# Kernel tuning notes

Hardware: AMD Instinct MI355X
Metric: run time of the kernel (lower is better)

## Reference

```python
import jax, jax.numpy as jnp
import numpy as np

EMBED_DIM = 1024
NUM_HEADS = 16
HEAD_DIM = EMBED_DIM // NUM_HEADS


def setup_inputs() -> dict:
    key = jax.random.key(0)
    k_x, k_wqkv, k_bqkv, k_wo, k_bo = jax.random.split(key, 5)
    B, T, C = 4, 2048, EMBED_DIM
    # PyTorch Linear default init scale ~ 1/sqrt(fan_in); use small normals
    s = 1.0 / np.sqrt(C)
    return {
        "x": jax.random.normal(k_x, (B, T, C), dtype=jnp.float32),
        "w_qkv": jax.random.normal(k_wqkv, (C, 3 * C), dtype=jnp.float32) * s,
        "b_qkv": jax.random.normal(k_bqkv, (3 * C,), dtype=jnp.float32) * s,
        "w_out": jax.random.normal(k_wo, (C, C), dtype=jnp.float32) * s,
        "b_out": jax.random.normal(k_bo, (C,), dtype=jnp.float32) * s,
    }


def reference(x, w_qkv, b_qkv, w_out, b_out):
    B, T, C = x.shape
    H, D = NUM_HEADS, HEAD_DIM
    qkv = x @ w_qkv + b_qkv                      # (B, T, 3C)
    q, k, v = jnp.split(qkv, 3, axis=-1)
    # (B, H, T, D)
    q = q.reshape(B, T, H, D).transpose(0, 2, 1, 3)
    k = k.reshape(B, T, H, D).transpose(0, 2, 1, 3)
    v = v.reshape(B, T, H, D).transpose(0, 2, 1, 3)
    scores = jnp.einsum("bhqd,bhkd->bhqk", q, k) / jnp.sqrt(jnp.float32(D))
    causal = jnp.tril(jnp.ones((T, T), dtype=bool))  # (T, T)
    scores = jnp.where(causal[None, None, :, :], scores, -jnp.inf)
    attn = jax.nn.softmax(scores, axis=-1)
    out = jnp.einsum("bhqk,bhkd->bhqd", attn, v)  # (B, H, T, D)
    out = out.transpose(0, 2, 1, 3).reshape(B, T, C)
    return out @ w_out + b_out
```

## Files before the change

kernel.cpp:

```cpp
#include <hip/hip_runtime.h>
#include <hip/hip_bf16.h>

#define B_  4
#define T_  2048
#define C_  1024
#define H_  16
#define D_  64
#define BH_ (B_*H_)

typedef float  f32x4  __attribute__((ext_vector_type(4)));
typedef __bf16 bf16x8 __attribute__((ext_vector_type(8)));
typedef __bf16 bf16x2 __attribute__((ext_vector_type(2)));

static __device__ __forceinline__ ushort f2bf(float f) {
    union { float f; unsigned u; } x; x.f = f;
    unsigned r = ((x.u >> 16) & 1u) + 0x7fffu;
    return (ushort)((x.u + r) >> 16);
}

static __device__ __forceinline__ uint packbf(float a, float b) {
    bf16x2 v = { (__bf16)a, (__bf16)b };
    return __builtin_bit_cast(uint, v);
}

static __device__ __forceinline__ void gload_lds16(const void* g, void* l) {
    __builtin_amdgcn_global_load_lds(
        (const __attribute__((address_space(1))) unsigned int*)g,
        (__attribute__((address_space(3))) unsigned int*)l, 16, 0, 0);
}

template<int N> static __device__ __forceinline__ void waitcnt_vm() {
    if constexpr (N == 0) asm volatile("s_waitcnt vmcnt(0)" ::: "memory");
    else if constexpr (N == 3) asm volatile("s_waitcnt vmcnt(3)" ::: "memory");
    else static_assert(N == 0 || N == 3);
    __builtin_amdgcn_sched_barrier(0);
}
static __device__ __forceinline__ void lgkm0() {
    asm volatile("s_waitcnt lgkmcnt(0)" ::: "memory");
    __builtin_amdgcn_sched_barrier(0);
}

__global__ __launch_bounds__(256) void prep_kernel(
    const float* __restrict__ x,     ushort* __restrict__ xb,
    const float* __restrict__ wqkv,  ushort* __restrict__ wqkvT,
    const float* __restrict__ wout,  ushort* __restrict__ woutT)
{
    __shared__ float tile[32][33];
    const int bid = blockIdx.x;
    if (bid < 8192) {
        int i = (bid * 256 + threadIdx.x) * 4;
        float4 v = *(const float4*)(x + i);
        ushort4 o;
        o.x = f2bf(v.x); o.y = f2bf(v.y); o.z = f2bf(v.z); o.w = f2bf(v.w);
        *(ushort4*)(xb + i) = o;
        return;
    }
    const float* in; ushort* out; int K, N, t;
    if (bid < 8192 + 3072) { t = bid - 8192;        in = wqkv; out = wqkvT; K = 1024; N = 3072; }
    else                   { t = bid - 8192 - 3072; in = wout; out = woutT; K = 1024; N = 1024; }
    const int nbx = N / 32;
    const int n0 = (t % nbx) * 32, k0 = (t / nbx) * 32;
    const int tx = threadIdx.x & 31, ty = threadIdx.x >> 5;
    #pragma unroll
    for (int r = 0; r < 32; r += 8)
        tile[ty + r][tx] = in[(size_t)(k0 + ty + r) * N + n0 + tx];
    __syncthreads();
    #pragma unroll
    for (int r = 0; r < 32; r += 8)
        out[(size_t)(n0 + ty + r) * K + k0 + tx] = f2bf(tile[tx][ty + r]);
}

template<int MFR, int NFR, bool QKV>
__global__ __launch_bounds__(512, 2) void gemm_hk(
    const ushort* __restrict__ A,
    const ushort* __restrict__ Bt,
    const float*  __restrict__ bias,
    void* __restrict__ outp,
    ushort* __restrict__ vtp)
{
    constexpr int NT    = 16;
    constexpr int BM    = MFR * 32;
    constexpr int BN    = NFR * 64;
    constexpr int APASS = BM / 128;
    constexpr int LB    = BN / 128;
    constexpr int ABUF  = BM * 128;
    constexpr int BBUF  = BN * 128;
    constexpr int PK    = APASS + LB;
    __shared__ __align__(16) char lds[2 * ABUF + 2 * BBUF];
    char* ldsB = lds + 2 * ABUF;

    const int gX   = gridDim.x;
    const int orig = blockIdx.y * gX + blockIdx.x;
    const int cpx  = (gX * gridDim.y) >> 3;
    const int wg   = (orig & 7) * cpx + (orig >> 3);
    const int m0 = (wg / gX) * BM, n0 = (wg % gX) * BN;

    const int tid = threadIdx.x, lane = tid & 63;
    const int wv = tid >> 6, wm = wv >> 2, wn = wv & 3;
    const int lr = lane & 15, lh = lane >> 4;

    const int sc = (tid & 3) ^ ((tid >> 2) & 3);
    const ushort* aA = A  + (size_t)(m0 + (tid >> 2)) * 1024 + sc * 8;
    const ushort* aB = Bt + (size_t)(n0 + (tid >> 2)) * 1024 + sc * 8;

    const int cxor = (lh ^ (lr & 3)) * 16;
    const int arow = (wm * (MFR * 16) + lr) * 64 + cxor;
    const int brow = (wn * (NFR * 16) + lr) * 64 + cxor;

    f32x4 acc[MFR][NFR] = {};

    auto stage_a = [&](int buf, int t, int kh) {
        #pragma unroll
        for (int p = 0; p < APASS; ++p)
            gload_lds16(aA + (size_t)p * 131072 + t * 64 + kh * 32,
                        lds + buf * ABUF + kh * (ABUF / 2) + p * 8192 + tid * 16);
    };
    auto stage_b = [&](int buf, int t, int kh) {
        #pragma unroll
        for (int p = 0; p < LB; ++p)
            gload_lds16(aB + (size_t)p * 131072 + t * 64 + kh * 32,
                        ldsB + buf * BBUF + kh * (BBUF / 2) + p * 8192 + tid * 16);
    };
    auto read_a = [&](bf16x8 (&af)[MFR], int buf, int kh) {
        const char* base = lds + buf * ABUF + kh * (ABUF / 2) + arow;
        #pragma unroll
        for (int mi = 0; mi < MFR; ++mi) af[mi] = *(const bf16x8*)(base + mi * 1024);
    };
    auto read_b = [&](bf16x8& b0, bf16x8& b1, int buf, int kh, int nh) {
        const char* base = ldsB + buf * BBUF + kh * (BBUF / 2) + brow + nh * 2048;
        b0 = *(const bf16x8*)(base);
        b1 = *(const bf16x8*)(base + 1024);
    };

#define MFMA2(NI, BB0, BB1)                                                          \
    do {                                                                             \
        __builtin_amdgcn_s_setprio(1);                                               \
        _Pragma("unroll")                                                            \
        for (int mi = 0; mi < MFR; ++mi) {                                           \
            acc[mi][NI]     = __builtin_amdgcn_mfma_f32_16x16x32_bf16(af[mi], BB0,   \
                                                     acc[mi][NI], 0, 0, 0);          \
            acc[mi][NI + 1] = __builtin_amdgcn_mfma_f32_16x16x32_bf16(af[mi], BB1,   \
                                                     acc[mi][NI + 1], 0, 0, 0);      \
        }                                                                            \
        __builtin_amdgcn_s_setprio(0);                                               \
    } while (0)

    stage_a(0, 0, 0); stage_b(0, 0, 0);
    stage_a(0, 0, 1); stage_b(0, 0, 1);
    waitcnt_vm<PK>();
    __builtin_amdgcn_s_barrier();

    for (int t = 0; t < NT; ++t) {
        const int cur = t & 1, nxt = cur ^ 1;
        const bool pf = (t + 1 < NT);
        bf16x8 af[MFR], b0, b1;
        read_a(af, cur, 0); read_b(b0, b1, cur, 0, 0);
        if (pf) { stage_a(nxt, t + 1, 0); stage_b(nxt, t + 1, 0); }
        if (t < NT - 1) waitcnt_vm<PK>(); else waitcnt_vm<0>();
        __builtin_amdgcn_s_barrier();
        lgkm0();
        MFMA2(0, b0, b1);
        read_a(af, cur, 1); read_b(b0, b1, cur, 1, 0);
        if (pf) { stage_a(nxt, t + 1, 1); stage_b(nxt, t + 1, 1); }
        if (t < NT - 1) waitcnt_vm<PK>();
        __builtin_amdgcn_s_barrier();
        lgkm0();
        MFMA2(0, b0, b1);
    }
#undef MFMA2

    #pragma unroll
    for (int mi = 0; mi < MFR; ++mi) {
        #pragma unroll
        for (int ni = 0; ni < NFR; ++ni) {
            int col = n0 + wn * (NFR * 16) + ni * 16 + lr;
            float bv = bias[col];
            if constexpr (QKV) {
                ushort* qkv = (ushort*)outp;
                int which = col >> 10;
                int h = (col & 1023) >> 6;
                int d = col & 63;
                if (which == 2) {
                    #pragma unroll
                    for (int r = 0; r < 4; ++r) {
                        int row = m0 + wm * (MFR * 16) + mi * 16 + lh * 4 + r;
                        int b = row >> 11, tt = row & 2047;
                        vtp[(((size_t)(b * H_ + h)) * D_ + d) * T_ + tt] =
                            f2bf(acc[mi][ni][r] + bv);
                    }
                } else {
                    #pragma unroll
                    for (int r = 0; r < 4; ++r) {
                        int row = m0 + wm * (MFR * 16) + mi * 16 + lh * 4 + r;
                        int b = row >> 11, tt = row & 2047;
                        float v = acc[mi][ni][r] + bv;
                        if (which == 0) v *= 0.18033688011112042f;
                        qkv[(size_t)which * (BH_ * T_ * D_) +
                            (((size_t)(b * H_ + h)) * T_ + tt) * D_ + d] = f2bf(v);
                    }
                }
            } else {
                float* Cout = (float*)outp;
                #pragma unroll
                for (int r = 0; r < 4; ++r) {
                    int row = m0 + wm * (MFR * 16) + mi * 16 + lh * 4 + r;
                    Cout[(size_t)row * C_ + col] = acc[mi][ni][r] + bv;
                }
            }
        }
    }
}

__global__ __launch_bounds__(256, 4) void flash_kernel(
    const ushort* __restrict__ qb,
    const ushort* __restrict__ kb,
    const ushort* __restrict__ vt,
    ushort* __restrict__ ob)
{
    __shared__ __align__(16) ushort sK[2][64 * 64];
    __shared__ __align__(16) ushort sV[2][64 * 64];
    const int wg  = ((blockIdx.x & 7) << 7) | (blockIdx.x >> 3);
    const int bh  = wg >> 4;
    const int pr  = wg & 15;
    const int qtA = pr, qtB = 31 - pr;
    const int lane = threadIdx.x & 63, wv = threadIdx.x >> 6;
    const int lr = lane & 15, lh = lane >> 4;

    const ushort* qrowA = qb + ((size_t)bh * T_ + qtA * 64 + wv * 16 + lr) * D_;
    const ushort* qrowB = qb + ((size_t)bh * T_ + qtB * 64 + wv * 16 + lr) * D_;
    bf16x8 qfA0 = *(const bf16x8*)(qrowA + lh * 8);
    bf16x8 qfA1 = *(const bf16x8*)(qrowA + 32 + lh * 8);
    bf16x8 qfB0 = *(const bf16x8*)(qrowB + lh * 8);
    bf16x8 qfB1 = *(const bf16x8*)(qrowB + 32 + lh * 8);

    const int srow = lane >> 3;
    const int scol = ((lane & 7) ^ srow) * 8;
    const ushort* kbase = kb + (size_t)bh * T_ * D_;
    const ushort* vbase = vt + (size_t)bh * D_ * T_;

    const int swv  = (lr & 7) << 4;
    const int off0 = (16 * lh) ^ swv;
    const int off1 = (64 + 16 * lh) ^ swv;

    f32x4 oA[4] = {}, oB[4] = {};
    float mA = -1e30f, lA = 0.f, mB = -1e30f, lB = 0.f;

    auto redmax = [&](float x) {
        x = fmaxf(x, __int_as_float(__builtin_amdgcn_ds_swizzle(__float_as_int(x), 0x401F)));
        x = fmaxf(x, __shfl_xor(x, 32, 64));
        return x;
    };
    auto redsum = [&](float x) {
        x += __int_as_float(__builtin_amdgcn_ds_swizzle(__float_as_int(x), 0x401F));
        x += __shfl_xor(x, 32, 64);
        return x;
    };

    auto maskS = [&](f32x4 (&s)[4]) {
        #pragma unroll
        for (int nt = 0; nt < 4; ++nt) {
            const int kb0 = 8 * lh + 4 * (nt & 1) + 32 * (nt >> 1);
            #pragma unroll
            for (int r = 0; r < 4; ++r)
                if (kb0 + r > wv * 16 + lr) s[nt][r] = -INFINITY;
        }
    };

    auto softmax_pv = [&](f32x4 (&s)[4], float& mrow, float& lsum, f32x4 (&o)[4],
                          const char* V0) {
        float t0 = fmaxf(fmaxf(s[0][0], s[0][1]), s[0][2]);
        float t1 = fmaxf(fmaxf(s[0][3], s[1][0]), s[1][1]);
        float t2 = fmaxf(fmaxf(s[1][2], s[1][3]), s[2][0]);
        float t3 = fmaxf(fmaxf(s[2][1], s[2][2]), s[2][3]);
        float t4 = fmaxf(fmaxf(s[3][0], s[3][1]), s[3][2]);
        float u0 = fmaxf(fmaxf(t0, t1), t2);
        float u1 = fmaxf(fmaxf(t3, t4), s[3][3]);
        float lmax = fmaxf(u0, u1);
        if (__any(lmax > mrow + 8.f)) {
            float pmax = redmax(lmax);
            float mnew = fmaxf(mrow, pmax);
            float al = __builtin_exp2f(mrow - mnew);
            lsum *= al;
            #pragma unroll
            for (int r = 0; r < 4; ++r) {
                float ar = __shfl(al, lh * 20 + r, 64);
                o[0][r] *= ar; o[1][r] *= ar; o[2][r] *= ar; o[3][r] *= ar;
            }
            mrow = mnew;
        }
        float rsum = 0.f;
        uint pk[8];
        #pragma unroll
        for (int nt = 0; nt < 4; ++nt) {
            float p0 = __builtin_exp2f(s[nt][0] - mrow);
            float p1 = __builtin_exp2f(s[nt][1] - mrow);
            float p2 = __builtin_exp2f(s[nt][2] - mrow);
            float p3 = __builtin_exp2f(s[nt][3] - mrow);
            rsum += (p0 + p1) + (p2 + p3);
            pk[nt * 2]     = packbf(p0, p1);
            pk[nt * 2 + 1] = packbf(p2, p3);
        }
        lsum += rsum;
        uint4 w0 = {pk[0], pk[1], pk[2], pk[3]};
        uint4 w1 = {pk[4], pk[5], pk[6], pk[7]};
        bf16x8 pf0 = __builtin_bit_cast(bf16x8, w0);
        bf16x8 pf1 = __builtin_bit_cast(bf16x8, w1);
        __builtin_amdgcn_s_setprio(1);
        #pragma unroll
        for (int dt = 0; dt < 4; ++dt) {
            const char* vrow = V0 + (dt * 16 + lr) * 128;
            bf16x8 v0 = *(const bf16x8*)(vrow + off0);
            bf16x8 v1 = *(const bf16x8*)(vrow + off1);
            o[dt] = __builtin_amdgcn_mfma_f32_16x16x32_bf16(pf0, v0, o[dt], 0, 0, 0);
            o[dt] = __builtin_amdgcn_mfma_f32_16x16x32_bf16(pf1, v1, o[dt], 0, 0, 0);
        }
        __builtin_amdgcn_s_setprio(0);
    };

    #pragma unroll
    for (int i = 0; i < 2; ++i) {
        int j = i * 4 + wv;
        gload_lds16(kbase + (size_t)(j * 8 + srow) * D_ + scol, &sK[0][j * 512]);
        gload_lds16(vbase + (size_t)(j * 8 + srow) * T_ + scol, &sV[0][j * 512]);
    }
    __syncthreads();

    for (int kt = 0; kt <= qtB; ++kt) {
        const int cur = kt & 1;
        if (kt < qtB) {
            const int nb = cur ^ 1;
            #pragma unroll
            for (int i = 0; i < 2; ++i) {
                int j = i * 4 + wv;
                gload_lds16(kbase + (size_t)((kt + 1) * 64 + j * 8 + srow) * D_ + scol, &sK[nb][j * 512]);
                gload_lds16(vbase + (size_t)(j * 8 + srow) * T_ + (kt + 1) * 64 + scol, &sV[nb][j * 512]);
            }
        }
        const bool doA = kt <= qtA;
        const char* K0 = (const char*)sK[cur];
        const char* V0 = (const char*)sV[cur];

        f32x4 sa[4], sb[4];
        __builtin_amdgcn_s_setprio(1);
        #pragma unroll
        for (int nt = 0; nt < 4; ++nt) {
            const int kk  = ((lr >> 2) << 3) | (lr & 3) | ((nt & 1) << 2) | ((nt >> 1) << 5);
            const int swk = (kk & 7) << 4;
            const char* krow = K0 + kk * 128;
            bf16x8 k0 = *(const bf16x8*)(krow + ((16 * lh) ^ swk));
            bf16x8 k1 = *(const bf16x8*)(krow + ((64 + 16 * lh) ^ swk));
            f32x4 a = {0.f, 0.f, 0.f, 0.f};
            a = __builtin_amdgcn_mfma_f32_16x16x32_bf16(k0, qfB0, a, 0, 0, 0);
            a = __builtin_amdgcn_mfma_f32_16x16x32_bf16(k1, qfB1, a, 0, 0, 0);
            sb[nt] = a;
            if (doA) {
                f32x4 c = {0.f, 0.f, 0.f, 0.f};
                c = __builtin_amdgcn_mfma_f32_16x16x32_bf16(k0, qfA0, c, 0, 0, 0);
                c = __builtin_amdgcn_mfma_f32_16x16x32_bf16(k1, qfA1, c, 0, 0, 0);
                sa[nt] = c;
            }
        }
        __builtin_amdgcn_s_setprio(0);
        if (kt == qtB) maskS(sb);
        if (doA && kt == qtA) maskS(sa);

        softmax_pv(sb, mB, lB, oB, V0);
        if (doA) softmax_pv(sa, mA, lA, oA, V0);
        __syncthreads();
    }

    const int b = bh >> 4, h = bh & 15;
    auto writeout = [&](f32x4 (&o)[4], float lsum, int q0) {
        float inv = 1.f / redsum(lsum);
        #pragma unroll
        for (int r = 0; r < 4; ++r) {
            float ir = __shfl(inv, lh * 20 + r, 64);
            int q = q0 + lh * 4 + r;
            #pragma unroll
            for (int dt = 0; dt < 4; ++dt)
                ob[((size_t)b * T_ + q) * C_ + h * 64 + dt * 16 + lr] = f2bf(o[dt][r] * ir);
        }
    };
    writeout(oA, lA, qtA * 64 + wv * 16);
    writeout(oB, lB, qtB * 64 + wv * 16);
}

extern "C" void kernel_launch(void* const* d_in, const int* in_sizes, int n_in,
                              void* d_out, int out_size, void* d_ws, size_t ws_size,
                              hipStream_t stream) {
    const float* x     = (const float*)d_in[0];
    const float* w_qkv = (const float*)d_in[1];
    const float* b_qkv = (const float*)d_in[2];
    const float* w_out = (const float*)d_in[3];
    const float* b_out = (const float*)d_in[4];
    float* out = (float*)d_out;

    char* ws = (char*)d_ws;
    ushort* xb     = (ushort*)(ws + 0);
    ushort* wqkvT  = (ushort*)(ws + 16777216);
    ushort* woutT  = (ushort*)(ws + 23068672);
    ushort* qkv    = (ushort*)(ws + 25165824);
    ushort* vT     = (ushort*)(ws + 75497472);
    ushort* attn   = xb;
    ushort* qb = qkv;
    ushort* kb = qkv + (size_t)BH_ * T_ * D_;

    prep_kernel<<<8192 + 3072 + 1024, 256, 0, stream>>>(x, xb, w_qkv, wqkvT, w_out, woutT);
    gemm_hk<8, 2, true><<<dim3(3 * C_ / 128, B_ * T_ / 256), 512, 0, stream>>>(xb, wqkvT, b_qkv, qkv, vT);
    flash_kernel<<<BH_ * 16, 256, 0, stream>>>(qb, kb, vT, attn);
    gemm_hk<8, 2, false><<<dim3(C_ / 128, B_ * T_ / 256), 512, 0, stream>>>(attn, woutT, b_out, out, nullptr);
}
```

Measured before the change: 190.2 us.

## Triple-buffer GEMM LDS pipeline and share V loads across both attention query tiles

The projection GEMM moves from double to triple buffering of its LDS tiles, prefetching two K-steps ahead with matching vmcnt waits, so global loads have more time to land. In the attention kernel, softmax is split from the PV product so the paired query tiles reuse the same V fragment reads in one interleaved MFMA loop. The cost is 50% more LDS per GEMM block, which may lower occupancy under launch_bounds(512,2), plus more live registers in attention. The hardcoded vmcnt values assume PK equals 3 for every instantiation.

Result: slower. 299.4 us (+57.4%).

```diff
diff --git a/kernel.cpp b/kernel.cpp
--- a/kernel.cpp
+++ b/kernel.cpp
@@ -32,7 +32,8 @@
 template<int N> static __device__ __forceinline__ void waitcnt_vm() {
     if constexpr (N == 0) asm volatile("s_waitcnt vmcnt(0)" ::: "memory");
     else if constexpr (N == 3) asm volatile("s_waitcnt vmcnt(3)" ::: "memory");
-    else static_assert(N == 0 || N == 3);
+    else if constexpr (N == 6) asm volatile("s_waitcnt vmcnt(6)" ::: "memory");
+    else static_assert(N == 0 || N == 3 || N == 6);
     __builtin_amdgcn_sched_barrier(0);
 }
 static __device__ __forceinline__ void lgkm0() {
@@ -85,9 +86,8 @@
     constexpr int LB    = BN / 128;
     constexpr int ABUF  = BM * 128;
     constexpr int BBUF  = BN * 128;
-    constexpr int PK    = APASS + LB;
-    __shared__ __align__(16) char lds[2 * ABUF + 2 * BBUF];
-    char* ldsB = lds + 2 * ABUF;
+    __shared__ __align__(16) char lds[3 * ABUF + 3 * BBUF];
+    char* ldsB = lds + 3 * ABUF;
 
     const int gX   = gridDim.x;
     const int orig = blockIdx.y * gX + blockIdx.x;
@@ -147,25 +147,31 @@
 
     stage_a(0, 0, 0); stage_b(0, 0, 0);
     stage_a(0, 0, 1); stage_b(0, 0, 1);
-    waitcnt_vm<PK>();
+    stage_a(1, 1, 0); stage_b(1, 1, 0);
+    stage_a(1, 1, 1); stage_b(1, 1, 1);
+    waitcnt_vm<6>();
     __builtin_amdgcn_s_barrier();
 
+    int cur = 0;
     for (int t = 0; t < NT; ++t) {
-        const int cur = t & 1, nxt = cur ^ 1;
-        const bool pf = (t + 1 < NT);
+        const int st = (cur + 2) % 3;
+        const bool pf = (t + 2 < NT);
         bf16x8 af[MFR], b0, b1;
         read_a(af, cur, 0); read_b(b0, b1, cur, 0, 0);
-        if (pf) { stage_a(nxt, t + 1, 0); stage_b(nxt, t + 1, 0); }
-        if (t < NT - 1) waitcnt_vm<PK>(); else waitcnt_vm<0>();
+        if (pf) { stage_a(st, t + 2, 0); stage_b(st, t + 2, 0); }
+        if (t < NT - 2) waitcnt_vm<6>();
+        else if (t == NT - 2) waitcnt_vm<3>();
         __builtin_amdgcn_s_barrier();
         lgkm0();
         MFMA2(0, b0, b1);
         read_a(af, cur, 1); read_b(b0, b1, cur, 1, 0);
-        if (pf) { stage_a(nxt, t + 1, 1); stage_b(nxt, t + 1, 1); }
-        if (t < NT - 1) waitcnt_vm<PK>();
+        if (pf) { stage_a(st, t + 2, 1); stage_b(st, t + 2, 1); }
+        if (t < NT - 2) waitcnt_vm<6>();
+        else if (t == NT - 2) waitcnt_vm<0>();
         __builtin_amdgcn_s_barrier();
         lgkm0();
         MFMA2(0, b0, b1);
+        cur = (cur + 1) % 3;
     }
 #undef MFMA2
 
@@ -266,8 +272,8 @@
         }
     };
 
-    auto softmax_pv = [&](f32x4 (&s)[4], float& mrow, float& lsum, f32x4 (&o)[4],
-                          const char* V0) {
+    auto softmax = [&](f32x4 (&s)[4], float& mrow, float& lsum, f32x4 (&o)[4],
+                       bf16x8& pf0, bf16x8& pf1) {
         float t0 = fmaxf(fmaxf(s[0][0], s[0][1]), s[0][2]);
         float t1 = fmaxf(fmaxf(s[0][3], s[1][0]), s[1][1]);
         float t2 = fmaxf(fmaxf(s[1][2], s[1][3]), s[2][0]);
@@ -303,18 +309,8 @@
         lsum += rsum;
         uint4 w0 = {pk[0], pk[1], pk[2], pk[3]};
         uint4 w1 = {pk[4], pk[5], pk[6], pk[7]};
-        bf16x8 pf0 = __builtin_bit_cast(bf16x8, w0);
-        bf16x8 pf1 = __builtin_bit_cast(bf16x8, w1);
-        __builtin_amdgcn_s_setprio(1);
-        #pragma unroll
-        for (int dt = 0; dt < 4; ++dt) {
-            const char* vrow = V0 + (dt * 16 + lr) * 128;
-            bf16x8 v0 = *(const bf16x8*)(vrow + off0);
-            bf16x8 v1 = *(const bf16x8*)(vrow + off1);
-            o[dt] = __builtin_amdgcn_mfma_f32_16x16x32_bf16(pf0, v0, o[dt], 0, 0, 0);
-            o[dt] = __builtin_amdgcn_mfma_f32_16x16x32_bf16(pf1, v1, o[dt], 0, 0, 0);
-        }
-        __builtin_amdgcn_s_setprio(0);
+        pf0 = __builtin_bit_cast(bf16x8, w0);
+        pf1 = __builtin_bit_cast(bf16x8, w1);
     };
 
     #pragma unroll
@@ -364,8 +360,35 @@
         if (kt == qtB) maskS(sb);
         if (doA && kt == qtA) maskS(sa);
 
-        softmax_pv(sb, mB, lB, oB, V0);
-        if (doA) softmax_pv(sa, mA, lA, oA, V0);
+        bf16x8 pfB0, pfB1;
+        softmax(sb, mB, lB, oB, pfB0, pfB1);
+        if (doA) {
+            bf16x8 pfA0, pfA1;
+            softmax(sa, mA, lA, oA, pfA0, pfA1);
+            __builtin_amdgcn_s_setprio(1);
+            #pragma unroll
+            for (int dt = 0; dt < 4; ++dt) {
+                const char* vrow = V0 + (dt * 16 + lr) * 128;
+                bf16x8 v0 = *(const bf16x8*)(vrow + off0);
+                bf16x8 v1 = *(const bf16x8*)(vrow + off1);
+                oB[dt] = __builtin_amdgcn_mfma_f32_16x16x32_bf16(pfB0, v0, oB[dt], 0, 0, 0);
+                oB[dt] = __builtin_amdgcn_mfma_f32_16x16x32_bf16(pfB1, v1, oB[dt], 0, 0, 0);
+                oA[dt] = __builtin_amdgcn_mfma_f32_16x16x32_bf16(pfA0, v0, oA[dt], 0, 0, 0);
+                oA[dt] = __builtin_amdgcn_mfma_f32_16x16x32_bf16(pfA1, v1, oA[dt], 0, 0, 0);
+            }
+            __builtin_amdgcn_s_setprio(0);
+        } else {
+            __builtin_amdgcn_s_setprio(1);
+            #pragma unroll
+            for (int dt = 0; dt < 4; ++dt) {
+                const char* vrow = V0 + (dt * 16 + lr) * 128;
+                bf16x8 v0 = *(const bf16x8*)(vrow + off0);
+                bf16x8 v1 = *(const bf16x8*)(vrow + off1);
+                oB[dt] = __builtin_amdgcn_mfma_f32_16x16x32_bf16(pfB0, v0, oB[dt], 0, 0, 0);
+                oB[dt] = __builtin_amdgcn_mfma_f32_16x16x32_bf16(pfB1, v1, oB[dt], 0, 0, 0);
+            }
+            __builtin_amdgcn_s_setprio(0);
+        }
         __syncthreads();
     }
 
```

## Restructure GEMM LDS staging to full-K tiles with two-ahead prefetch

Applied to the files above, without the earlier changes.

The GEMM main loop now stages each full 64-wide K slice of A and B into LDS in one go, with an 8-chunk XOR swizzle replacing the split half-K layout. Two tiles are prefetched ahead and the wait uses vmcnt(6), so one tile's loads overlap the compute on the other. The explicit lgkmcnt waits are removed and the barriers are moved around the compute. The aim is fewer barriers per K step and deeper overlap of global loads with MFMA work. The catch is less slack between issuing a load and using it, and the compiler now has to insert the LDS-read waits itself.

Measured after the change: 183.1 us. 3.8% less time.

```diff
diff --git a/kernel.cpp b/kernel.cpp
--- a/kernel.cpp
+++ b/kernel.cpp
@@ -31,12 +31,8 @@
 
 template<int N> static __device__ __forceinline__ void waitcnt_vm() {
     if constexpr (N == 0) asm volatile("s_waitcnt vmcnt(0)" ::: "memory");
-    else if constexpr (N == 3) asm volatile("s_waitcnt vmcnt(3)" ::: "memory");
-    else static_assert(N == 0 || N == 3);
-    __builtin_amdgcn_sched_barrier(0);
-}
-static __device__ __forceinline__ void lgkm0() {
-    asm volatile("s_waitcnt lgkmcnt(0)" ::: "memory");
+    else if constexpr (N == 6) asm volatile("s_waitcnt vmcnt(6)" ::: "memory");
+    else static_assert(N == 0 || N == 6);
     __builtin_amdgcn_sched_barrier(0);
 }
 
@@ -81,11 +77,10 @@
     constexpr int NT    = 16;
     constexpr int BM    = MFR * 32;
     constexpr int BN    = NFR * 64;
-    constexpr int APASS = BM / 128;
-    constexpr int LB    = BN / 128;
+    constexpr int APASS = BM / 64;
+    constexpr int BPASS = BN / 64;
     constexpr int ABUF  = BM * 128;
     constexpr int BBUF  = BN * 128;
-    constexpr int PK    = APASS + LB;
     __shared__ __align__(16) char lds[2 * ABUF + 2 * BBUF];
     char* ldsB = lds + 2 * ABUF;
 
@@ -99,73 +94,68 @@
     const int wv = tid >> 6, wm = wv >> 2, wn = wv & 3;
     const int lr = lane & 15, lh = lane >> 4;
 
-    const int sc = (tid & 3) ^ ((tid >> 2) & 3);
-    const ushort* aA = A  + (size_t)(m0 + (tid >> 2)) * 1024 + sc * 8;
-    const ushort* aB = Bt + (size_t)(n0 + (tid >> 2)) * 1024 + sc * 8;
-
-    const int cxor = (lh ^ (lr & 3)) * 16;
-    const int arow = (wm * (MFR * 16) + lr) * 64 + cxor;
-    const int brow = (wn * (NFR * 16) + lr) * 64 + cxor;
+    const int dchunk = (tid & 7) ^ ((tid >> 3) & 7);
+    const ushort* aA = A  + (size_t)(m0 + (tid >> 3)) * 1024 + dchunk * 8;
+    const ushort* aB = Bt + (size_t)(n0 + (tid >> 3)) * 1024 + dchunk * 8;
+
+    const int axor0 = ((0 + lh) ^ (lr & 7)) * 16;
+    const int axor1 = ((4 + lh) ^ (lr & 7)) * 16;
 
     f32x4 acc[MFR][NFR] = {};
 
-    auto stage_a = [&](int buf, int t, int kh) {
+    auto stage = [&](int buf, int t) {
         #pragma unroll
         for (int p = 0; p < APASS; ++p)
-            gload_lds16(aA + (size_t)p * 131072 + t * 64 + kh * 32,
-                        lds + buf * ABUF + kh * (ABUF / 2) + p * 8192 + tid * 16);
-    };
-    auto stage_b = [&](int buf, int t, int kh) {
-        #pragma unroll
-        for (int p = 0; p < LB; ++p)
-            gload_lds16(aB + (size_t)p * 131072 + t * 64 + kh * 32,
-                        ldsB + buf * BBUF + kh * (BBUF / 2) + p * 8192 + tid * 16);
+            gload_lds16(aA + (size_t)p * 65536 + t * 64,
+                        lds + buf * ABUF + p * 8192 + tid * 16);
+        #pragma unroll
+        for (int p = 0; p < BPASS; ++p)
+            gload_lds16(aB + (size_t)p * 65536 + t * 64,
+                        ldsB + buf * BBUF + p * 8192 + tid * 16);
     };
     auto read_a = [&](bf16x8 (&af)[MFR], int buf, int kh) {
-        const char* base = lds + buf * ABUF + kh * (ABUF / 2) + arow;
-        #pragma unroll
-        for (int mi = 0; mi < MFR; ++mi) af[mi] = *(const bf16x8*)(base + mi * 1024);
-    };
-    auto read_b = [&](bf16x8& b0, bf16x8& b1, int buf, int kh, int nh) {
-        const char* base = ldsB + buf * BBUF + kh * (BBUF / 2) + brow + nh * 2048;
+        const char* base = lds + buf * ABUF + (wm * (MFR * 16) + lr) * 128
+                               + (kh ? axor1 : axor0);
+        #pragma unroll
+        for (int mi = 0; mi < MFR; ++mi) af[mi] = *(const bf16x8*)(base + mi * 2048);
+    };
+    auto read_b = [&](bf16x8& b0, bf16x8& b1, int buf, int kh) {
+        const char* base = ldsB + buf * BBUF + (wn * (NFR * 16) + lr) * 128
+                                + (kh ? axor1 : axor0);
         b0 = *(const bf16x8*)(base);
-        b1 = *(const bf16x8*)(base + 1024);
-    };
-
-#define MFMA2(NI, BB0, BB1)                                                          \
+        b1 = *(const bf16x8*)(base + 2048);
+    };
+
+#define MFMA2(BB0, BB1)                                                              \
     do {                                                                             \
         __builtin_amdgcn_s_setprio(1);                                               \
         _Pragma("unroll")                                                            \
         for (int mi = 0; mi < MFR; ++mi) {                                           \
-            acc[mi][NI]     = __builtin_amdgcn_mfma_f32_16x16x32_bf16(af[mi], BB0,   \
-                                                     acc[mi][NI], 0, 0, 0);          \
-            acc[mi][NI + 1] = __builtin_amdgcn_mfma_f32_16x16x32_bf16(af[mi], BB1,   \
-                                                     acc[mi][NI + 1], 0, 0, 0);      \
+            acc[mi][0] = __builtin_amdgcn_mfma_f32_16x16x32_bf16(af[mi], BB0,        \
+                                                     acc[mi][0], 0, 0, 0);           \
+            acc[mi][1] = __builtin_amdgcn_mfma_f32_16x16x32_bf16(af[mi], BB1,        \
+                                                     acc[mi][1], 0, 0, 0);           \
         }                                                                            \
         __builtin_amdgcn_s_setprio(0);                                               \
     } while (0)
 
-    stage_a(0, 0, 0); stage_b(0, 0, 0);
-    stage_a(0, 0, 1); stage_b(0, 0, 1);
-    waitcnt_vm<PK>();
-    __builtin_amdgcn_s_barrier();
+    stage(0, 0);
+    stage(1, 1);
 
     for (int t = 0; t < NT; ++t) {
-        const int cur = t & 1, nxt = cur ^ 1;
-        const bool pf = (t + 1 < NT);
+        const int cur = t & 1;
+        if (t < NT - 1) waitcnt_vm<6>();
+        else            waitcnt_vm<0>();
+        __builtin_amdgcn_s_barrier();
+
         bf16x8 af[MFR], b0, b1;
-        read_a(af, cur, 0); read_b(b0, b1, cur, 0, 0);
-        if (pf) { stage_a(nxt, t + 1, 0); stage_b(nxt, t + 1, 0); }
-        if (t < NT - 1) waitcnt_vm<PK>(); else waitcnt_vm<0>();
+        read_a(af, cur, 0); read_b(b0, b1, cur, 0);
+        MFMA2(b0, b1);
+        read_a(af, cur, 1); read_b(b0, b1, cur, 1);
+        MFMA2(b0, b1);
+
         __builtin_amdgcn_s_barrier();
-        lgkm0();
-        MFMA2(0, b0, b1);
-        read_a(af, cur, 1); read_b(b0, b1, cur, 1, 0);
-        if (pf) { stage_a(nxt, t + 1, 1); stage_b(nxt, t + 1, 1); }
-        if (t < NT - 1) waitcnt_vm<PK>();
-        __builtin_amdgcn_s_barrier();
-        lgkm0();
-        MFMA2(0, b0, b1);
+        if (t + 2 < NT) stage(cur, t + 2);
     }
 #undef MFMA2
 
```
